# Performance work log

Measured on AMD Instinct MI355X. Metric: run time of the kernel, lower is better.

Reference implementation:

```python
import jax, jax.numpy as jnp
import numpy as np

EMB = 3          # embedding_size
NSIG = 1         # n_sigma
FG_W = 1.0       # foreground_weight
W_INST, W_VAR, W_SEED = 1.0, 10.0, 1.0
K_MAX = 8        # fixed number of instance ids (1..K_MAX); 0 is background


def _xyzm(T, H, W):
    # buffer is linspace over the FULL grid (32,800,2000), then sliced
    t = jnp.linspace(0.0, 0.1, 32)[:T]
    y = jnp.linspace(0.0, 1.6, 800)[:H]
    x = jnp.linspace(0.0, 4.16, 2000)[:W]
    tt = jnp.broadcast_to(t[:, None, None], (T, H, W))
    yy = jnp.broadcast_to(y[None, :, None], (T, H, W))
    xx = jnp.broadcast_to(x[None, None, :], (T, H, W))
    return jnp.stack([tt, yy, xx], 0)  # [3,T,H,W]


def _lovasz_hinge_flat(logits, labels):
    # standard Berman lovasz hinge on flat [N] logits/labels (labels in {0,1})
    signs = 2.0 * labels - 1.0
    errors = 1.0 - logits * signs
    order = jnp.argsort(-errors)             # descending errors
    errors_sorted = errors[order]
    gt_sorted = labels[order]
    gts = gt_sorted.sum()
    inter = gts - jnp.cumsum(gt_sorted)
    union = gts + jnp.cumsum(1.0 - gt_sorted)
    jac = 1.0 - inter / union
    grad = jnp.concatenate([jac[:1], jac[1:] - jac[:-1]])
    return jnp.dot(jax.nn.relu(errors_sorted), jax.lax.stop_gradient(grad))


def _forward(prediction, instances):
    B, C, T, H, W = prediction.shape
    xyzm = _xyzm(T, H, W).astype(prediction.dtype)

    emb = jnp.tanh(prediction[:, :EMB])                 # [B,3,T,H,W]
    spatial = emb + xyzm[None]                          # spatial_emb
    sigma = prediction[:, EMB]                          # [B,T,H,W] (n_sigma=1)
    seed = jax.nn.sigmoid(prediction[:, EMB + NSIG])    # [B,T,H,W]

    ids = jnp.arange(1, K_MAX + 1)
    masks = (instances[:, None] == ids[None, :, None, None, None]).astype(prediction.dtype)  # [B,K,T,H,W]
    counts = masks.sum((2, 3, 4))                       # [B,K]
    present = (counts > 0).astype(prediction.dtype)
    safe = jnp.maximum(counts, 1.0)

    # per-instance center of xyzm (to_center=True) and mean sigma
    centers = jnp.einsum('cthw,bkthw->bkc', xyzm, masks) / safe[..., None]   # [B,K,3]
    s_mean = jnp.einsum('bthw,bkthw->bk', sigma, masks) / safe               # [B,K]
    s_sg = jax.lax.stop_gradient(s_mean)

    # var loss: mean over mask of (sigma - stop_grad(s_mean))^2
    sig2 = jnp.einsum('bthw,bkthw->bk', sigma * sigma, masks) / safe
    var_k = sig2 - 2.0 * s_sg * s_mean + s_sg * s_sg                          # [B,K]

    # gaussian distance map: exp(-s * ||spatial - center||^2)
    s_exp = jnp.exp(s_mean * 10.0)                                            # [B,K]
    e2 = jnp.sum(spatial * spatial, axis=1)                                   # [B,T,H,W]
    ec = jnp.einsum('bcthw,bkc->bkthw', spatial, centers)                     # [B,K,T,H,W]
    c2 = jnp.sum(centers * centers, axis=-1)                                  # [B,K]
    sqdist = e2[:, None] - 2.0 * ec + c2[:, :, None, None, None]
    dist = jnp.exp(-s_exp[:, :, None, None, None] * sqdist)                   # [B,K,T,H,W]

    # lovasz hinge per instance
    logits = (dist * 2.0 - 1.0).reshape(B * K_MAX, -1)
    labels_flat = masks.reshape(B * K_MAX, -1)
    inst_k = jax.vmap(_lovasz_hinge_flat)(logits, labels_flat).reshape(B, K_MAX)

    obj = present.sum(1)
    safe_obj = jnp.maximum(obj, 1.0)
    inst_loss = (inst_k * present).sum(1) / safe_obj
    var_loss = (var_k * present).sum(1) / safe_obj

    # seed loss: background -> 0, foreground -> stop_grad(dist)
    bg = (instances == 0).astype(prediction.dtype)
    seed_bg = jnp.sum(bg * seed * seed, axis=(1, 2, 3))
    dsg = jax.lax.stop_gradient(dist)
    seed_fg = FG_W * jnp.sum(masks * (seed[:, None] - dsg) ** 2, axis=(1, 2, 3, 4))
    seed_loss = (seed_bg + seed_fg) / (H * W)

    return jnp.mean(W_INST * inst_loss + W_VAR * var_loss + W_SEED * seed_loss)


def setup_inputs() -> dict:
    key = jax.random.key(0)
    k1, k2, k3 = jax.random.split(key, 3)
    prediction = jax.random.normal(k1, (2, 5, 8, 256, 512), dtype=jnp.float32)
    instances = jax.random.randint(k2, (2, 8, 256, 512), 0, 9, dtype=jnp.int32)
    labels = jax.random.randint(k3, (2, 8, 256, 512), 0, 2, dtype=jnp.int32)
    return {"prediction": prediction, "instances": instances, "labels": labels}


def reference(prediction, instances, labels):
    # `labels` is accepted by the torch forward but unused in the loss math
    return _forward(prediction, instances)
```

## Files before the change

### kernel.cpp

```cpp
#include <hip/hip_runtime.h>
#include <math.h>

#define BB 2
#define KK 8
#define NB 256
#define HALF_NB_F 128.0f
#define FAR_CUT 5.545177444479562f

#define PXB_H 2048
#define GRID_H 1024
#define PXB_A 2048
#define GRID_A 1024
#define NPART_A 512

#define STEP_T (0.1f/31.0f)
#define STEP_Y (1.6f/799.0f)
#define STEP_X (4.16f/1999.0f)

#define OFF_CNT 0
#define OFF_PRM 32
#define OFF_GH2 512
#define OFF_PARTA 9216
#define OFF_SEED2 59392
#define OFF_HIST_F 65536

typedef float nvf4 __attribute__((ext_vector_type(4)));
typedef int   nvi4 __attribute__((ext_vector_type(4)));

__device__ __forceinline__ float4 ntload4f(const float* p) {
  nvf4 v = __builtin_nontemporal_load((const nvf4*)p);
  return make_float4(v.x, v.y, v.z, v.w);
}
__device__ __forceinline__ int4 ntload4i(const int* p) {
  nvi4 v = __builtin_nontemporal_load((const nvi4*)p);
  return make_int4(v.x, v.y, v.z, v.w);
}

__global__ __launch_bounds__(256) void k_acc(const float* __restrict__ pred,
                                             const int* __restrict__ inst,
                                             float* __restrict__ ws) {
  int tid = threadIdx.x, blk = blockIdx.x;
  int b = blk >> 9;
  int rbase = (blk & 511) * PXB_A;
  const float* sig_p = pred + ((size_t)b * 5 << 20) + (3 << 20);
  const int* ip = inst + ((size_t)b << 20);
  float acc[48];
  #pragma unroll
  for (int f = 0; f < 48; ++f) acc[f] = 0.f;
  #pragma unroll
  for (int it = 0; it < 2; ++it) {
    int r = rbase + it * 1024 + 4 * tid;
    float4 sg4 = ntload4f(sig_p + r);
    int4 id4 = ntload4i(ip + r);
    float tf = (float)(r >> 17), hf = (float)((r >> 9) & 255), wf = (float)(r & 511);
    float sv[4] = {sg4.x, sg4.y, sg4.z, sg4.w};
    int iv[4] = {id4.x, id4.y, id4.z, id4.w};
    #pragma unroll
    for (int j = 0; j < 4; ++j) {
      #pragma unroll
      for (int k = 0; k < KK; ++k) {
        float m = (iv[j] == k + 1) ? 1.f : 0.f;
        acc[k*6+0] += m;
        acc[k*6+1] += m * sv[j];
        acc[k*6+2] += m * sv[j] * sv[j];
        acc[k*6+3] += m * tf;
        acc[k*6+4] += m * hf;
        acc[k*6+5] += m * (wf + (float)j);
      }
    }
  }
  __shared__ float lds[4 * 48];
  int lane = tid & 63, wv = tid >> 6;
  #pragma unroll
  for (int f = 0; f < 48; ++f) {
    float v = acc[f];
    for (int o = 32; o; o >>= 1) v += __shfl_down(v, o);
    if (lane == 0) lds[wv * 48 + f] = v;
  }
  __syncthreads();
  if (tid < 48)
    ws[OFF_PARTA + ((size_t)b * 48 + tid) * NPART_A + (blk & 511)]
      = lds[tid] + lds[48 + tid] + lds[96 + tid] + lds[144 + tid];
}

__global__ __launch_bounds__(256) void k_params(float* __restrict__ ws) {
  __shared__ float accs[96];
  int tid = threadIdx.x;
  if (tid < 96) {
    const float* p = ws + OFF_PARTA + (size_t)tid * NPART_A;
    float s0 = 0.f, s1 = 0.f, s2 = 0.f, s3 = 0.f;
    for (int j = 0; j < NPART_A; j += 4) {
      s0 += p[j]; s1 += p[j+1]; s2 += p[j+2]; s3 += p[j+3];
    }
    accs[tid] = (s0 + s1) + (s2 + s3);
  }
  __syncthreads();
  if (tid < 16) {
    float* a = &accs[(tid >> 3) * 48 + (tid & 7) * 6];
    float cnt = a[0], s1 = a[1], s2 = a[2], st = a[3], sy = a[4], sx = a[5];
    float safe = fmaxf(cnt, 1.f);
    float smean = s1 / safe;
    float A = __expf(10.f * smean);
    float ct = st * STEP_T / safe;
    float cy = sy * STEP_Y / safe;
    float cx = sx * STEP_X / safe;
    ws[OFF_CNT + tid] = cnt;
    ws[OFF_PRM + tid*8 + 0] = 2.f * A * ct;
    ws[OFF_PRM + tid*8 + 1] = 2.f * A * cy;
    ws[OFF_PRM + tid*8 + 2] = 2.f * A * cx;
    ws[OFF_PRM + tid*8 + 3] = A;
    ws[OFF_PRM + tid*8 + 4] = A * (ct*ct + cy*cy + cx*cx);
    ws[OFF_PRM + tid*8 + 5] = s2 / safe - smean * smean;
    ws[OFF_PRM + tid*8 + 6] = (cnt > 0.f) ? 1.f : 0.f;
    ws[OFF_PRM + tid*8 + 7] = 0.f;
  }
}

__device__ __forceinline__ float fast_tanh(float x) {
  x = fminf(fmaxf(x, -15.f), 15.f);
  float ex = __expf(2.f * x);
  return (ex - 1.f) / (ex + 1.f);
}

__global__ __launch_bounds__(512, 8) void k_hist(const float* __restrict__ pred,
                                                 const int* __restrict__ inst,
                                                 float* __restrict__ ws) {
  __shared__ unsigned int hist[KK * NB];
  __shared__ float Ps[KK * 8];
  __shared__ float wred[16];
  int tid = threadIdx.x;
  int blk = blockIdx.x;
  int b = blk >> 9;
  for (int i = tid; i < KK * NB; i += 512) hist[i] = 0u;
  if (tid < KK * 8) Ps[tid] = ws[OFF_PRM + b * 64 + tid];
  __syncthreads();
  unsigned pmask = 0;
  #pragma unroll
  for (int k = 0; k < KK; ++k) if (Ps[k*8 + 6] > 0.f) pmask |= 1u << k;
  int r = (blk & 511) * PXB_H + 4 * tid;
  const float* pb = pred + ((size_t)b * 5 << 20);
  float tf = (float)(r >> 17), hf = (float)((r >> 9) & 255);
  int w = r & 511;
  float4 p0 = ntload4f(pb + r);
  float4 p1 = ntload4f(pb + (1 << 20) + r);
  float4 p2 = ntload4f(pb + (2 << 20) + r);
  float4 p4 = ntload4f(pb + (4 << 20) + r);
  int4 id4 = ntload4i(inst + ((size_t)b << 20) + r);
  int iv[4] = {id4.x, id4.y, id4.z, id4.w};
  float e0[4], e1[4], e2[4], ee[4], sd[4];
  {
    float q0[4] = {p0.x,p0.y,p0.z,p0.w}, q1[4] = {p1.x,p1.y,p1.z,p1.w};
    float q2[4] = {p2.x,p2.y,p2.z,p2.w}, q4[4] = {p4.x,p4.y,p4.z,p4.w};
    #pragma unroll
    for (int j = 0; j < 4; ++j) {
      e0[j] = fast_tanh(q0[j]) + tf * STEP_T;
      e1[j] = fast_tanh(q1[j]) + hf * STEP_Y;
      e2[j] = fast_tanh(q2[j]) + (float)(w + j) * STEP_X;
      ee[j] = e0[j]*e0[j] + e1[j]*e1[j] + e2[j]*e2[j];
      sd[j] = 1.f / (1.f + __expf(-q4[j]));
    }
  }
  float sbg = 0.f, sfg = 0.f;
  #pragma unroll
  for (int j = 0; j < 4; ++j) if (iv[j] == 0) sbg += sd[j] * sd[j];
  int lane = tid & 63;
  unsigned hot[KK];
  #pragma unroll
  for (int k = 0; k < KK; ++k) hot[k] = 0u;
  #pragma unroll
  for (int k = 0; k < KK; ++k) {
    if (!((pmask >> k) & 1)) continue;
    float Bt = Ps[k*8+0], By = Ps[k*8+1], Bx = Ps[k*8+2], A = Ps[k*8+3], C = Ps[k*8+4];
    #pragma unroll
    for (int j = 0; j < 4; ++j) {
      float ssq = fmaf(-Bt, e0[j], fmaf(-By, e1[j], fmaf(-Bx, e2[j], fmaf(A, ee[j], C))));
      bool lab = (iv[j] == k + 1);
      bool skip = (ssq >= FAR_CUT) && !lab;
      unsigned long long ms = __ballot(skip);
      hot[k] += (unsigned)__popcll(ms);
      if (!skip) {
        float d = __expf(-ssq);
        if (lab) { float df = sd[j] - d; sfg += df * df; }
        float e = lab ? (2.f - 2.f * d) : (2.f * d);
        int bin = min((int)(e * HALF_NB_F), NB - 1);
        atomicAdd(&hist[k * NB + bin], lab ? 0x10000u : 1u);
      }
    }
  }
  if (lane == 0) {
    #pragma unroll
    for (int k = 0; k < KK; ++k)
      if (hot[k]) atomicAdd(&hist[k * NB], hot[k]);
  }
  for (int off = 32; off; off >>= 1) {
    sbg += __shfl_down(sbg, off);
    sfg += __shfl_down(sfg, off);
  }
  if (lane == 0) { wred[(tid >> 6) * 2] = sbg; wred[(tid >> 6) * 2 + 1] = sfg; }
  __syncthreads();
  if (tid == 0) {
    float b0 = 0.f, f0 = 0.f;
    #pragma unroll
    for (int v = 0; v < 8; ++v) { b0 += wred[v*2]; f0 += wred[v*2+1]; }
    ((float2*)(ws + OFF_SEED2))[blk] = make_float2(b0, f0);
  }
  uint4* gp = (uint4*)((unsigned int*)(ws + OFF_HIST_F) + (size_t)blk * (KK * NB));
  gp[tid] = ((const uint4*)hist)[tid];
}

__global__ __launch_bounds__(256) void k_red(float* __restrict__ ws) {
  int blk = blockIdx.x;
  int tid = threadIdx.x;
  int seg = blk >> 4, range = blk & 15;
  int b = seg >> 3, k = seg & 7;
  __shared__ unsigned long long sred[256];
  int bin_off = tid & 15;
  int pgrp = tid >> 4;
  const unsigned int* gh = (const unsigned int*)(ws + OFF_HIST_F);
  size_t base = ((size_t)b * 512 + (size_t)pgrp * 32) * (KK * NB)
              + (size_t)k * NB + (size_t)range * 16 + bin_off;
  unsigned int neg = 0, pos = 0;
  #pragma unroll 4
  for (int j = 0; j < 32; ++j) {
    unsigned v = gh[base + (size_t)j * (KK * NB)];
    neg += v & 0xFFFFu; pos += v >> 16;
  }
  sred[tid] = ((unsigned long long)pos << 32) | neg;
  __syncthreads();
  if (tid < 16) {
    unsigned long long a = 0;
    #pragma unroll
    for (int j = 0; j < 16; ++j) a += sred[tid + j * 16];
    ((unsigned long long*)(ws + OFF_GH2))[seg * NB + range * 16 + tid] = a;
  }
}

__global__ __launch_bounds__(256) void k_fin(float* __restrict__ ws, float* __restrict__ out) {
  int tid = threadIdx.x;
  int lane = tid & 63, wv = tid >> 6;
  __shared__ double segtot[16];
  __shared__ float sdb[4], sdf[4];
  {
    const float2* sp = (const float2*)(ws + OFF_SEED2);
    float sb = 0.f, sf = 0.f;
    #pragma unroll
    for (int j = 0; j < 4; ++j) { float2 v = sp[tid * 4 + j]; sb += v.x; sf += v.y; }
    for (int o = 32; o; o >>= 1) { sb += __shfl_down(sb, o); sf += __shfl_down(sf, o); }
    if (lane == 0) { sdb[wv] = sb; sdf[wv] = sf; }
  }
  const unsigned long long* gh2 = (const unsigned long long*)(ws + OFF_GH2);
  for (int s = wv; s < 16; s += 4) {
    double total = 0.0;
    if (ws[OFF_PRM + s*8 + 6] != 0.f) {
      double gts = (double)ws[OFF_CNT + s];
      unsigned long long carry = 0;
      double sum = 0.0;
      for (int c = 0; c < NB / 64; ++c) {
        int bin = NB - 1 - (c * 64 + lane);
        unsigned long long v = gh2[s * NB + bin];
        unsigned long long orig = v;
        #pragma unroll
        for (int o = 1; o < 64; o <<= 1) {
          unsigned long long u = (unsigned long long)__shfl_up((long long)v, o, 64);
          if (lane >= o) v += u;
        }
        v += carry;
        if (orig) {
          unsigned int ip = (unsigned)(v >> 32), in_ = (unsigned)v;
          unsigned int ppx = (unsigned)(orig >> 32), nnx = (unsigned)orig;
          double ep = (double)(ip - ppx), en = (double)(in_ - nnx);
          double js = 1.0 - (gts - ep) / (gts + en);
          double je = 1.0 - (gts - (double)ip) / (gts + (double)in_);
          sum += ((double)bin + 0.5) * (2.0 / NB) * (je - js);
        }
        carry = (unsigned long long)__shfl((long long)v, 63, 64);
      }
      for (int o = 32; o; o >>= 1) sum += __shfl_down(sum, o);
      total = sum;
    }
    if (lane == 0) segtot[s] = total;
  }
  __syncthreads();
  if (tid == 0) {
    double tot = 0.0;
    for (int bb = 0; bb < BB; ++bb) {
      double il = 0.0, vl = 0.0, ob = 0.0;
      for (int k2 = 0; k2 < KK; ++k2) {
        int s2 = bb * 8 + k2;
        double pr = (double)ws[OFF_PRM + s2*8 + 6];
        il += segtot[s2] * pr;
        vl += (double)ws[OFF_PRM + s2*8 + 5] * pr;
        ob += pr;
      }
      double so = (ob > 1.0) ? ob : 1.0;
      double sbg = (double)sdb[bb * 2] + (double)sdb[bb * 2 + 1];
      double sfg = (double)sdf[bb * 2] + (double)sdf[bb * 2 + 1];
      tot += il / so + 10.0 * vl / so + (sbg + sfg) / (256.0 * 512.0);
    }
    out[0] = (float)(tot / BB);
  }
}

extern "C" void kernel_launch(void* const* d_in, const int* in_sizes, int n_in,
                              void* d_out, int out_size, void* d_ws, size_t ws_size,
                              hipStream_t stream) {
  const float* pred = (const float*)d_in[0];
  const int* inst = (const int*)d_in[1];
  float* ws = (float*)d_ws;
  float* out = (float*)d_out;
  k_acc<<<GRID_A, 256, 0, stream>>>(pred, inst, ws);
  k_params<<<1, 256, 0, stream>>>(ws);
  k_hist<<<GRID_H, 512, 0, stream>>>(pred, inst, ws);
  k_red<<<256, 256, 0, stream>>>(ws);
  k_fin<<<1, 256, 0, stream>>>(ws, out);
}
```

Baseline: 146.2 us.

## Fuse parameter kernel into histogram kernel and coarsen accumulation partials

Removes the single-block k_params launch. Every k_hist block now reduces the per-instance partials itself and computes its centers and seed parameters in shared memory. k_acc uses fewer, larger blocks, cutting the partial count from 512 to 128 per field so that redundant per-block reduction stays cheap. The far-cut path now handles labelled pixels too, routing positives to the top bin and adding sd^2 to the foreground seed term, and replaces per-pixel ballots with one wave shuffle reduction per instance. The cost is redundant parameter computation in each of 1024 blocks and lower occupancy in k_acc.

```diff
diff --git a/kernel.cpp b/kernel.cpp
--- a/kernel.cpp
+++ b/kernel.cpp
@@ -9,9 +9,8 @@
 
 #define PXB_H 2048
 #define GRID_H 1024
-#define PXB_A 2048
-#define GRID_A 1024
-#define NPART_A 512
+#define GRID_A 256
+#define NPART_A 128
 
 #define STEP_T (0.1f/31.0f)
 #define STEP_Y (1.6f/799.0f)
@@ -21,8 +20,8 @@
 #define OFF_PRM 32
 #define OFF_GH2 512
 #define OFF_PARTA 9216
-#define OFF_SEED2 59392
-#define OFF_HIST_F 65536
+#define OFF_SEED2 25600
+#define OFF_HIST_F 32768
 
 typedef float nvf4 __attribute__((ext_vector_type(4)));
 typedef int   nvi4 __attribute__((ext_vector_type(4)));
@@ -36,20 +35,20 @@
   return make_int4(v.x, v.y, v.z, v.w);
 }
 
-__global__ __launch_bounds__(256) void k_acc(const float* __restrict__ pred,
+__global__ __launch_bounds__(512) void k_acc(const float* __restrict__ pred,
                                              const int* __restrict__ inst,
                                              float* __restrict__ ws) {
   int tid = threadIdx.x, blk = blockIdx.x;
-  int b = blk >> 9;
-  int rbase = (blk & 511) * PXB_A;
+  int b = blk >> 7;
+  int rbase = (blk & 127) * 8192;
   const float* sig_p = pred + ((size_t)b * 5 << 20) + (3 << 20);
   const int* ip = inst + ((size_t)b << 20);
   float acc[48];
   #pragma unroll
   for (int f = 0; f < 48; ++f) acc[f] = 0.f;
   #pragma unroll
-  for (int it = 0; it < 2; ++it) {
-    int r = rbase + it * 1024 + 4 * tid;
+  for (int it = 0; it < 4; ++it) {
+    int r = rbase + it * 2048 + 4 * tid;
     float4 sg4 = ntload4f(sig_p + r);
     int4 id4 = ntload4i(ip + r);
     float tf = (float)(r >> 17), hf = (float)((r >> 9) & 255), wf = (float)(r & 511);
@@ -69,7 +68,7 @@
       }
     }
   }
-  __shared__ float lds[4 * 48];
+  __shared__ float lds[8 * 48];
   int lane = tid & 63, wv = tid >> 6;
   #pragma unroll
   for (int f = 0; f < 48; ++f) {
@@ -78,25 +77,48 @@
     if (lane == 0) lds[wv * 48 + f] = v;
   }
   __syncthreads();
-  if (tid < 48)
-    ws[OFF_PARTA + ((size_t)b * 48 + tid) * NPART_A + (blk & 511)]
-      = lds[tid] + lds[48 + tid] + lds[96 + tid] + lds[144 + tid];
-}
-
-__global__ __launch_bounds__(256) void k_params(float* __restrict__ ws) {
-  __shared__ float accs[96];
+  if (tid < 48) {
+    float s = 0.f;
+    #pragma unroll
+    for (int w8 = 0; w8 < 8; ++w8) s += lds[w8 * 48 + tid];
+    ws[OFF_PARTA + ((size_t)b * 48 + tid) * NPART_A + (blk & 127)] = s;
+  }
+}
+
+__device__ __forceinline__ float fast_tanh(float x) {
+  x = fminf(fmaxf(x, -15.f), 15.f);
+  float ex = __expf(2.f * x);
+  return (ex - 1.f) / (ex + 1.f);
+}
+
+__global__ __launch_bounds__(512, 8) void k_hist(const float* __restrict__ pred,
+                                                 const int* __restrict__ inst,
+                                                 float* __restrict__ ws) {
+  __shared__ unsigned int hist[KK * NB];
+  __shared__ float fred[48 * 8];
+  __shared__ float accs[48];
+  __shared__ float Ps[KK * 8];
+  __shared__ float wred[16];
   int tid = threadIdx.x;
-  if (tid < 96) {
-    const float* p = ws + OFF_PARTA + (size_t)tid * NPART_A;
-    float s0 = 0.f, s1 = 0.f, s2 = 0.f, s3 = 0.f;
-    for (int j = 0; j < NPART_A; j += 4) {
-      s0 += p[j]; s1 += p[j+1]; s2 += p[j+2]; s3 += p[j+3];
-    }
-    accs[tid] = (s0 + s1) + (s2 + s3);
-  }
-  __syncthreads();
-  if (tid < 16) {
-    float* a = &accs[(tid >> 3) * 48 + (tid & 7) * 6];
+  int blk = blockIdx.x;
+  int b = blk >> 9;
+  for (int i = tid; i < KK * NB; i += 512) hist[i] = 0u;
+  if (tid < 384) {
+    int f = tid >> 3, g = tid & 7;
+    const float* p = ws + OFF_PARTA + ((size_t)b * 48 + f) * NPART_A + g * 16;
+    float s = 0.f;
+    #pragma unroll
+    for (int j = 0; j < 16; ++j) s += p[j];
+    fred[f * 8 + g] = s;
+  }
+  __syncthreads();
+  if (tid < 48) {
+    const float* q = &fred[tid * 8];
+    accs[tid] = ((q[0]+q[1])+(q[2]+q[3])) + ((q[4]+q[5])+(q[6]+q[7]));
+  }
+  __syncthreads();
+  if (tid < 8) {
+    const float* a = &accs[tid * 6];
     float cnt = a[0], s1 = a[1], s2 = a[2], st = a[3], sy = a[4], sx = a[5];
     float safe = fmaxf(cnt, 1.f);
     float smean = s1 / safe;
@@ -104,39 +126,25 @@
     float ct = st * STEP_T / safe;
     float cy = sy * STEP_Y / safe;
     float cx = sx * STEP_X / safe;
-    ws[OFF_CNT + tid] = cnt;
-    ws[OFF_PRM + tid*8 + 0] = 2.f * A * ct;
-    ws[OFF_PRM + tid*8 + 1] = 2.f * A * cy;
-    ws[OFF_PRM + tid*8 + 2] = 2.f * A * cx;
-    ws[OFF_PRM + tid*8 + 3] = A;
-    ws[OFF_PRM + tid*8 + 4] = A * (ct*ct + cy*cy + cx*cx);
-    ws[OFF_PRM + tid*8 + 5] = s2 / safe - smean * smean;
-    ws[OFF_PRM + tid*8 + 6] = (cnt > 0.f) ? 1.f : 0.f;
-    ws[OFF_PRM + tid*8 + 7] = 0.f;
-  }
-}
-
-__device__ __forceinline__ float fast_tanh(float x) {
-  x = fminf(fmaxf(x, -15.f), 15.f);
-  float ex = __expf(2.f * x);
-  return (ex - 1.f) / (ex + 1.f);
-}
-
-__global__ __launch_bounds__(512, 8) void k_hist(const float* __restrict__ pred,
-                                                 const int* __restrict__ inst,
-                                                 float* __restrict__ ws) {
-  __shared__ unsigned int hist[KK * NB];
-  __shared__ float Ps[KK * 8];
-  __shared__ float wred[16];
-  int tid = threadIdx.x;
-  int blk = blockIdx.x;
-  int b = blk >> 9;
-  for (int i = tid; i < KK * NB; i += 512) hist[i] = 0u;
-  if (tid < KK * 8) Ps[tid] = ws[OFF_PRM + b * 64 + tid];
+    float var = s2 / safe - smean * smean;
+    float pres = (cnt > 0.f) ? 1.f : 0.f;
+    Ps[tid*8 + 0] = 2.f * A * ct;
+    Ps[tid*8 + 1] = 2.f * A * cy;
+    Ps[tid*8 + 2] = 2.f * A * cx;
+    Ps[tid*8 + 3] = A;
+    Ps[tid*8 + 4] = A * (ct*ct + cy*cy + cx*cx);
+    Ps[tid*8 + 5] = pres;
+    if ((blk & 511) == 0) {
+      int seg = b * 8 + tid;
+      ws[OFF_CNT + seg] = cnt;
+      ws[OFF_PRM + seg*8 + 5] = var;
+      ws[OFF_PRM + seg*8 + 6] = pres;
+    }
+  }
   __syncthreads();
   unsigned pmask = 0;
   #pragma unroll
-  for (int k = 0; k < KK; ++k) if (Ps[k*8 + 6] > 0.f) pmask |= 1u << k;
+  for (int k = 0; k < KK; ++k) if (Ps[k*8 + 5] > 0.f) pmask |= 1u << k;
   int r = (blk & 511) * PXB_H + 4 * tid;
   const float* pb = pred + ((size_t)b * 5 << 20);
   float tf = (float)(r >> 17), hf = (float)((r >> 9) & 255);
@@ -175,22 +183,28 @@
     for (int j = 0; j < 4; ++j) {
       float ssq = fmaf(-Bt, e0[j], fmaf(-By, e1[j], fmaf(-Bx, e2[j], fmaf(A, ee[j], C))));
       bool lab = (iv[j] == k + 1);
-      bool skip = (ssq >= FAR_CUT) && !lab;
-      unsigned long long ms = __ballot(skip);
-      hot[k] += (unsigned)__popcll(ms);
-      if (!skip) {
+      if (ssq >= FAR_CUT) {
+        hot[k] += lab ? 0x10000u : 1u;
+        if (lab) sfg += sd[j] * sd[j];
+      } else {
         float d = __expf(-ssq);
-        if (lab) { float df = sd[j] - d; sfg += df * df; }
-        float e = lab ? (2.f - 2.f * d) : (2.f * d);
+        float e;
+        if (lab) { float df = sd[j] - d; sfg += df * df; e = 2.f - 2.f * d; }
+        else e = 2.f * d;
         int bin = min((int)(e * HALF_NB_F), NB - 1);
         atomicAdd(&hist[k * NB + bin], lab ? 0x10000u : 1u);
       }
     }
   }
-  if (lane == 0) {
-    #pragma unroll
-    for (int k = 0; k < KK; ++k)
-      if (hot[k]) atomicAdd(&hist[k * NB], hot[k]);
+  #pragma unroll
+  for (int k = 0; k < KK; ++k) {
+    unsigned v = hot[k];
+    for (int o = 32; o; o >>= 1) v += __shfl_down(v, o);
+    if (lane == 0 && v) {
+      unsigned neg = v & 0xFFFFu, pos = v & 0xFFFF0000u;
+      if (neg) atomicAdd(&hist[k * NB], neg);
+      if (pos) atomicAdd(&hist[k * NB + NB - 1], pos);
+    }
   }
   for (int off = 32; off; off >>= 1) {
     sbg += __shfl_down(sbg, off);
@@ -308,8 +322,7 @@
   const int* inst = (const int*)d_in[1];
   float* ws = (float*)d_ws;
   float* out = (float*)d_out;
-  k_acc<<<GRID_A, 256, 0, stream>>>(pred, inst, ws);
-  k_params<<<1, 256, 0, stream>>>(ws);
+  k_acc<<<GRID_A, 512, 0, stream>>>(pred, inst, ws);
   k_hist<<<GRID_H, 512, 0, stream>>>(pred, inst, ws);
   k_red<<<256, 256, 0, stream>>>(ws);
   k_fin<<<1, 256, 0, stream>>>(ws, out);
```

Measured after the change: 137.4 us, median of 2. 6.0% less time.
